# Kernel tuning notes

Measured on AMD Instinct MI355X. Metric: run time of the kernel, lower is better.

The kernel has to match this reference:

```python
import jax, jax.numpy as jnp
import numpy as np

HD = 128; ED = 64; V = 11; K = 64; L = 1024; LQ = 1024
EPS = 1e-5

def _ln(x, g, b):
    m = jnp.mean(x, axis=-1, keepdims=True)
    v = jnp.mean((x - m) ** 2, axis=-1, keepdims=True)
    return (x - m) / jnp.sqrt(v + EPS) * g + b

def _conv1d(x, w, b):
    # x: [B, C, L], w: [O, I, 3] (torch Conv1d layout), padding=1
    y = jax.lax.conv_general_dilated(x, w, (1,), [(1, 1)],
                                     dimension_numbers=("NCH", "OIH", "NCH"))
    return y + b[None, :, None]

def _enc(ids, emb, c1w, c1b, c2w, c2b, c3w, c3b, n1g, n1b, n2g, n2b, n3g, n3b):
    h = emb[ids].transpose(0, 2, 1)                      # [B, ED, L]
    h = jax.nn.relu(_conv1d(h, c1w, c1b)).transpose(0, 2, 1)
    h = _ln(h, n1g, n1b).transpose(0, 2, 1)
    h = jax.nn.relu(_conv1d(h, c2w, c2b)).transpose(0, 2, 1)
    h = _ln(h, n2g, n2b).transpose(0, 2, 1)
    h = jax.nn.relu(_conv1d(h, c3w, c3b)).transpose(0, 2, 1)
    return _ln(h, n3g, n3b)                              # [B, L, HD]

def setup_inputs() -> dict:
    key = jax.random.key(0)
    ks = iter(jax.random.split(key, 64))
    def nrm(shape, s=0.05):
        return (jax.random.normal(next(ks), shape, dtype=jnp.float32) * s)
    inp = {
        "support_inputs": jax.random.randint(next(ks), (K, L), 0, 10),
        "support_outputs": jax.random.randint(next(ks), (K, L), 0, 10),
        "query_input": jax.random.randint(next(ks), (LQ,), 0, 10),
    }
    for pre in ("qe", "se"):
        inp[pre + "_emb"] = nrm((V, ED)).at[10].set(0.0)
        inp[pre + "_c1w"] = nrm((HD, ED, 3)); inp[pre + "_c1b"] = nrm((HD,))
        inp[pre + "_c2w"] = nrm((HD, HD, 3)); inp[pre + "_c2b"] = nrm((HD,))
        inp[pre + "_c3w"] = nrm((HD, HD, 3)); inp[pre + "_c3b"] = nrm((HD,))
        for i in (1, 2, 3):
            inp[pre + f"_n{i}g"] = jnp.ones((HD,), jnp.float32)
            inp[pre + f"_n{i}b"] = jnp.zeros((HD,), jnp.float32)
    inp["out_emb"] = nrm((V, HD)).at[10].set(0.0)
    inp["dec_w1"] = nrm((HD, 2 * HD)); inp["dec_b1"] = nrm((HD,))
    inp["dec_lng"] = jnp.ones((HD,), jnp.float32)
    inp["dec_lnb"] = jnp.zeros((HD,), jnp.float32)
    inp["dec_w2"] = nrm((10, HD)); inp["dec_b2"] = nrm((10,))
    return inp

def reference(support_inputs, support_outputs, query_input,
              qe_emb, qe_c1w, qe_c1b, qe_c2w, qe_c2b, qe_c3w, qe_c3b,
              qe_n1g, qe_n1b, qe_n2g, qe_n2b, qe_n3g, qe_n3b,
              se_emb, se_c1w, se_c1b, se_c2w, se_c2b, se_c3w, se_c3b,
              se_n1g, se_n1b, se_n2g, se_n2b, se_n3g, se_n3b,
              out_emb, dec_w1, dec_b1, dec_lng, dec_lnb, dec_w2, dec_b2):
    q = _enc(query_input[None], qe_emb, qe_c1w, qe_c1b, qe_c2w, qe_c2b,
             qe_c3w, qe_c3b, qe_n1g, qe_n1b, qe_n2g, qe_n2b, qe_n3g, qe_n3b)[0]   # [LQ, HD]
    s = _enc(support_inputs, se_emb, se_c1w, se_c1b, se_c2w, se_c2b,
             se_c3w, se_c3b, se_n1g, se_n1b, se_n2g, se_n2b, se_n3g, se_n3b)      # [K, L, HD]
    keys = s.reshape(-1, HD)                              # [K*L, HD]
    values = out_emb[support_outputs].reshape(-1, HD)     # [K*L, HD]
    scores = (q @ keys.T) / jnp.sqrt(jnp.float32(HD))     # [LQ, K*L]
    attn = jax.nn.softmax(scores, axis=-1)
    attended = attn @ values                              # [LQ, HD]
    combined = jnp.concatenate([q, attended], axis=-1)    # [LQ, 2*HD]
    h = jax.nn.relu(combined @ dec_w1.T + dec_b1)
    h = _ln(h, dec_lng, dec_lnb)
    return h @ dec_w2.T + dec_b2                          # [LQ, 10]
```

## Files before the change

kernel.cpp:

```cpp
#include <hip/hip_runtime.h>


typedef __attribute__((ext_vector_type(8))) short short8;
typedef __attribute__((ext_vector_type(4))) float f32x4;
typedef __attribute__((ext_vector_type(4))) int int4v;
typedef __attribute__((ext_vector_type(4))) _Float16 half4;

#define EPSV 1e-5f
#define SC 0.12751676f

__device__ __forceinline__ float b2f(unsigned short u) {
  union { unsigned int i; float f; } v; v.i = ((unsigned int)u) << 16; return v.f;
}
__device__ __forceinline__ unsigned short f2b(float f) {
  union { float f; unsigned int i; } v; v.f = f;
  unsigned int r = v.i + 0x7fffu + ((v.i >> 16) & 1u);
  return (unsigned short)(r >> 16);
}
__device__ __forceinline__ f32x4 mfma32(short8 a, short8 b, f32x4 c) {
  return __builtin_amdgcn_mfma_f32_16x16x32_bf16(a, b, c, 0, 0, 0);
}
__device__ __forceinline__ f32x4 mfma16(half4 a, half4 b, f32x4 c) {
  return __builtin_amdgcn_mfma_f32_16x16x16f16(a, b, c, 0, 0, 0);
}
__device__ __forceinline__ void gl_lds16(const void* g, void* l) {
  __builtin_amdgcn_global_load_lds(
      (const __attribute__((address_space(1))) void*)g,
      (__attribute__((address_space(3))) void*)l, 16, 0, 0);
}
__device__ __forceinline__ half4 exp4_pk(f32x4 c) {
  float x0 = exp2f(c[0] * SC - 4.0f), x1 = exp2f(c[1] * SC - 4.0f);
  float x2 = exp2f(c[2] * SC - 4.0f), x3 = exp2f(c[3] * SC - 4.0f);
  union { __fp16 __attribute__((ext_vector_type(2))) h; unsigned int u; } a, b;
  a.h = __builtin_amdgcn_cvt_pkrtz(x0, x1);
  b.h = __builtin_amdgcn_cvt_pkrtz(x2, x3);
  union { unsigned int u[2]; half4 v; } r;
  r.u[0] = a.u; r.u[1] = b.u;
  return r.v;
}

#define OFF_WQ1 0
#define OFF_WQ2 24576
#define OFF_WQ3 73728
#define OFF_WS1 122880
#define OFF_WS2 147456
#define OFF_WS3 196608
#define OFF_EMBQ 245760
#define OFF_EMBS 246464
#define OFF_PBQ 247168
#define OFF_PBS 248320
#define OFF_OEMB 249472
#define OFF_DW1 250880
#define OFF_DB1 283648
#define OFF_DLNG 283776
#define OFF_DLNB 283904
#define OFF_DW2 284032
#define OFF_DB2 285312

__global__ __launch_bounds__(256) void mn_prep(
    const void* qc1w, const void* qc2w, const void* qc3w,
    const void* sc1w, const void* sc2w, const void* sc3w,
    const void* qemb, const void* semb,
    const void* qc1b, const void* qc2b, const void* qc3b,
    const void* qn1g, const void* qn1b, const void* qn2g, const void* qn2b,
    const void* qn3g, const void* qn3b,
    const void* sc1b, const void* sc2b, const void* sc3b,
    const void* sn1g, const void* sn1b, const void* sn2g, const void* sn2b,
    const void* sn3g, const void* sn3b,
    const void* oemb, const void* dw1, const void* db1, const void* dlng,
    const void* dlnb, const void* dw2, const void* db2,
    unsigned short* __restrict__ P, const unsigned int* __restrict__ det) {
  const bool f32m = (*det == 0x3F800000u);
  const int j = blockIdx.y;
  const void* src; int off, n, cin;
  switch (j) {
    case 0:  src = qc1w; off = OFF_WQ1; n = 24576; cin = 64; break;
    case 1:  src = qc2w; off = OFF_WQ2; n = 49152; cin = 128; break;
    case 2:  src = qc3w; off = OFF_WQ3; n = 49152; cin = 128; break;
    case 3:  src = sc1w; off = OFF_WS1; n = 24576; cin = 64; break;
    case 4:  src = sc2w; off = OFF_WS2; n = 49152; cin = 128; break;
    case 5:  src = sc3w; off = OFF_WS3; n = 49152; cin = 128; break;
    case 6:  src = qemb; off = OFF_EMBQ; n = 704; cin = 0; break;
    case 7:  src = semb; off = OFF_EMBS; n = 704; cin = 0; break;
    case 8:  src = qc1b; off = OFF_PBQ + 0; n = 128; cin = 0; break;
    case 9:  src = qc2b; off = OFF_PBQ + 128; n = 128; cin = 0; break;
    case 10: src = qc3b; off = OFF_PBQ + 256; n = 128; cin = 0; break;
    case 11: src = qn1g; off = OFF_PBQ + 384; n = 128; cin = 0; break;
    case 12: src = qn1b; off = OFF_PBQ + 512; n = 128; cin = 0; break;
    case 13: src = qn2g; off = OFF_PBQ + 640; n = 128; cin = 0; break;
    case 14: src = qn2b; off = OFF_PBQ + 768; n = 128; cin = 0; break;
    case 15: src = qn3g; off = OFF_PBQ + 896; n = 128; cin = 0; break;
    case 16: src = qn3b; off = OFF_PBQ + 1024; n = 128; cin = 0; break;
    case 17: src = sc1b; off = OFF_PBS + 0; n = 128; cin = 0; break;
    case 18: src = sc2b; off = OFF_PBS + 128; n = 128; cin = 0; break;
    case 19: src = sc3b; off = OFF_PBS + 256; n = 128; cin = 0; break;
    case 20: src = sn1g; off = OFF_PBS + 384; n = 128; cin = 0; break;
    case 21: src = sn1b; off = OFF_PBS + 512; n = 128; cin = 0; break;
    case 22: src = sn2g; off = OFF_PBS + 640; n = 128; cin = 0; break;
    case 23: src = sn2b; off = OFF_PBS + 768; n = 128; cin = 0; break;
    case 24: src = sn3g; off = OFF_PBS + 896; n = 128; cin = 0; break;
    case 25: src = sn3b; off = OFF_PBS + 1024; n = 128; cin = 0; break;
    case 26: src = oemb; off = OFF_OEMB; n = 1408; cin = 0; break;
    case 27: src = dw1; off = OFF_DW1; n = 32768; cin = 0; break;
    case 28: src = db1; off = OFF_DB1; n = 128; cin = 0; break;
    case 29: src = dlng; off = OFF_DLNG; n = 128; cin = 0; break;
    case 30: src = dlnb; off = OFF_DLNB; n = 128; cin = 0; break;
    case 31: src = dw2; off = OFF_DW2; n = 1280; cin = 0; break;
    default: src = db2; off = OFF_DB2; n = 10; cin = 0; break;
  }
  for (int e = blockIdx.x * 256 + threadIdx.x; e < n; e += gridDim.x * 256) {
    int si = e;
    if (cin) {
      int kw = 3 * cin;
      int o = e / kw, rem = e - o * kw;
      int c = rem >> 3, s = rem & 7;
      int k = ((c ^ (o & 7)) << 3) + s;
      int t = k / cin, i = k - t * cin;
      si = o * kw + i * 3 + t;
    }
    unsigned short v = f32m ? f2b(((const float*)src)[si]) : ((const unsigned short*)src)[si];
    P[off + e] = v;
  }
}

__global__ __launch_bounds__(256) void mn_gtf16(const int* __restrict__ so,
                                                unsigned short* __restrict__ gtf) {
  int t = blockIdx.x * 256 + threadIdx.x;
  int kb = t >> 6, l = t & 63;
  int id = l & 15, g = l >> 4;
  const int* base = so + kb * 16 + g * 4;
  half4 v;
#pragma unroll
  for (int j = 0; j < 4; ++j) {
    int s = base[j];
    bool on = (id < 11) ? (s == id) : (id == 11);
    v[j] = on ? (_Float16)1.0f : (_Float16)0.0f;
  }
  *(half4*)(gtf + (size_t)t * 4) = v;
}

template <int CIN, bool EMBED>
__global__ __launch_bounds__(256, 1) void mn_conv(
    const int* __restrict__ sup_ids, const int* __restrict__ q_ids,
    const unsigned short* __restrict__ in_act,
    const unsigned short* __restrict__ se_emb, const unsigned short* __restrict__ qe_emb,
    const unsigned short* __restrict__ se_wt, const unsigned short* __restrict__ qe_wt,
    const unsigned short* __restrict__ se_b, const unsigned short* __restrict__ qe_b,
    const unsigned short* __restrict__ se_g, const unsigned short* __restrict__ qe_g,
    const unsigned short* __restrict__ se_bt, const unsigned short* __restrict__ qe_bt,
    unsigned short* __restrict__ out_act) {
  constexpr int RB = CIN * 2;
  constexpr int KW = 3 * CIN;
  constexpr int RWB = KW * 2;
  constexpr int WB = 128 * RWB;
  constexpr int XB = 130 * RB;
  constexpr int NK = KW / 32;
  constexpr int WIT = WB / 4096;
  constexpr int CH = RB / 16;
  constexpr int NTASK = 130 * CH;
  constexpr int NT = (NTASK + 255) / 256;
  __shared__ __attribute__((aligned(16))) char lds[WB + XB + 4 * 4352];

  const int b = blockIdx.x;
  int first, nitems;
  if (b < 244)      { first = 2 * b;             nitems = 2; }
  else if (b < 252) { first = 488 + 3 * (b - 244); nitems = 3; }
  else              { first = 512 + 2 * (b - 252); nitems = 2; }
  const bool is_q = (first >= 512);

  const int tid = threadIdx.x;
  const int l = tid & 63, w = tid >> 6;
  const unsigned short* wt = is_q ? qe_wt : se_wt;
  const unsigned short* bs = is_q ? qe_b : se_b;
  const unsigned short* gg = is_q ? qe_g : se_g;
  const unsigned short* bt = is_q ? qe_bt : se_bt;
  const unsigned short* emb = is_q ? qe_emb : se_emb;
  char* xlds = lds + WB;

  {
    const char* wsrc = (const char*)wt + (size_t)(w * WIT) * 1024 + l * 16;
    char* wdst = lds + (w * WIT) * 1024;
#pragma unroll
    for (int i = 0; i < WIT; ++i) gl_lds16(wsrc + i * 1024, wdst + i * 1024);
  }

  int4v vals[NT];
  int dsto[NT];
#define XPHASE1(ITEM)                                                          \
  do {                                                                         \
    int _seq = (ITEM) >> 3, _t0 = ((ITEM) & 7) * 128;                          \
    const int* _ids = EMBED ? (is_q ? q_ids : (sup_ids + _seq * 1024)) : nullptr; \
    const unsigned short* _src = EMBED ? nullptr : in_act + (size_t)_seq * 1024 * CIN; \
    _Pragma("unroll") for (int i = 0; i < NT; ++i) {                           \
      int task = tid + i * 256;                                                \
      int r = task / CH, cb = (task % CH) * 16;                                \
      int p = _t0 + r - 1;                                                     \
      bool ok = (task < NTASK) && p >= 0 && p < 1024;                          \
      int4v v = {0, 0, 0, 0};                                                  \
      if constexpr (EMBED) {                                                   \
        if (ok) v = *(const int4v*)((const char*)emb + _ids[p] * RB + cb);     \
      } else {                                                                 \
        if (ok) v = *(const int4v*)((const char*)_src + (size_t)p * RB + cb);  \
      }                                                                        \
      vals[i] = v;                                                             \
      dsto[i] = (task < NTASK) ? (r * RB + (cb ^ ((r & 7) << 4))) : -1;        \
    }                                                                          \
  } while (0)
#define XPHASE2                                                                \
  do {                                                                         \
    _Pragma("unroll") for (int i = 0; i < NT; ++i)                             \
      if (dsto[i] >= 0) *(int4v*)(xlds + dsto[i]) = vals[i];                   \
  } while (0)

  XPHASE1(first);
  XPHASE2;
  asm volatile("s_waitcnt vmcnt(0)" ::: "memory");
  __syncthreads();

  const int g = l >> 4, q16 = l & 15;
  const int pbase = w * 32;

  float pb[8], pg[8], pt_[8];
#pragma unroll
  for (int ob = 0; ob < 8; ++ob) {
    int o = ob * 16 + q16;
    pb[ob] = b2f(bs[o]); pg[ob] = b2f(gg[o]); pt_[ob] = b2f(bt[o]);
  }
  char* wrep = lds + WB + XB + w * 4352;

  for (int s = 0; s < nitems; ++s) {
    const int item = first + s;
    const int seqI = item >> 3, t0I = (item & 7) * 128;

    f32x4 acc[2][8];
#pragma unroll
    for (int pt = 0; pt < 2; ++pt)
#pragma unroll
      for (int ob = 0; ob < 8; ++ob) acc[pt][ob] = (f32x4){0.f, 0.f, 0.f, 0.f};

#pragma unroll
    for (int ks = 0; ks < NK; ++ks) {
      const int kk = ks * 32;
      const int t = kk / CIN, i0 = kk % CIN;
      const int cb = (i0 + g * 8) * 2;
      short8 a0, a1;
      {
        int r = pbase + q16 + t;
        a0 = *(const short8*)(xlds + r * RB + (cb ^ ((r & 7) << 4)));
        r += 16;
        a1 = *(const short8*)(xlds + r * RB + (cb ^ ((r & 7) << 4)));
      }
      const int wc = ((ks * 4 + g) ^ (q16 & 7)) << 4;
#pragma unroll
      for (int ob = 0; ob < 8; ++ob) {
        short8 bb = *(const short8*)(lds + (ob * 16 + q16) * RWB + wc);
        acc[0][ob] = mfma32(a0, bb, acc[0][ob]);
        acc[1][ob] = mfma32(a1, bb, acc[1][ob]);
      }
    }
    __syncthreads();

    const bool more = (s + 1 < nitems);
    if (more) XPHASE1(item + 1);

#pragma unroll
    for (int pt = 0; pt < 2; ++pt) {
#pragma unroll
      for (int rg = 0; rg < 4; ++rg) {
        float v[8], sm = 0.f, sq = 0.f;
#pragma unroll
        for (int ob = 0; ob < 8; ++ob) {
          float x = acc[pt][ob][rg] + pb[ob];
          x = fmaxf(x, 0.f);
          v[ob] = x; sm += x; sq += x * x;
        }
#pragma unroll
        for (int m = 1; m < 16; m <<= 1) {
          sm += __shfl_xor(sm, m);
          sq += __shfl_xor(sq, m);
        }
        float mean = sm * (1.f / 128.f);
        float var = sq * (1.f / 128.f) - mean * mean;
        float rstd = rsqrtf(var + EPSV);
        unsigned short* dst = (unsigned short*)(wrep + (g * 4 + rg) * 272);
#pragma unroll
        for (int ob = 0; ob < 8; ++ob)
          dst[ob * 16 + q16] = f2b((v[ob] - mean) * rstd * pg[ob] + pt_[ob]);
      }
      char* obase = (char*)out_act + ((size_t)seqI * 1024 + t0I + pbase + pt * 16) * 256;
#pragma unroll
      for (int i = 0; i < 4; ++i) {
        int task = i * 64 + l;
        int pos = task >> 4, chk = task & 15;
        int4v v = *(const int4v*)(wrep + pos * 272 + chk * 16);
        *(int4v*)(obase + pos * 256 + chk * 16) = v;
      }
    }

    if (more) {
      XPHASE2;
      __syncthreads();
    }
  }
#undef XPHASE1
#undef XPHASE2
}

__global__ __launch_bounds__(256, 2) void mn_attn(const unsigned short* __restrict__ act3,
                                                  const unsigned short* __restrict__ gtf,
                                                  float* __restrict__ Hp) {
  __shared__ __attribute__((aligned(16))) char smem[27648];
  const int tid = threadIdx.x;
  const int l = tid & 63, w = tid >> 6;
  const int g = l >> 4, q16 = l & 15;
  const int ch = blockIdx.x;
  const int qt0 = (blockIdx.y * 4 + w) * 2;

  short8 qfa[4], qfb[4];
  const unsigned short* qrow = act3 + ((size_t)(64 * 1024 + qt0 * 16 + q16)) * 128;
#pragma unroll
  for (int ks = 0; ks < 4; ++ks) {
    qfa[ks] = *(const short8*)(qrow + ks * 32 + g * 8);
    qfb[ks] = *(const short8*)(qrow + 16 * 128 + ks * 32 + g * 8);
  }

  const char* kglob = (const char*)act3 + ((size_t)ch * 1024) * 256;
  const char* gglob = (const char*)gtf + ((size_t)ch * 64) * 512;

  int o0 = (w * 2) * 64 + l, o1 = (w * 2 + 1) * 64 + l;
  int r0s = o0 >> 4, c0s = (o0 & 15) ^ (r0s & 7);
  int r1s = o1 >> 4, c1s = (o1 & 15) ^ (r1s & 7);

#define STAGE(BUF, T)                                                          \
  do {                                                                         \
    const char* _gk = kglob + (size_t)(T) * 8192;                              \
    char* _lk = smem + (BUF) * 8192;                                           \
    gl_lds16(_gk + r0s * 256 + c0s * 16, _lk + (w * 2) * 1024);                \
    gl_lds16(_gk + r1s * 256 + c1s * 16, _lk + (w * 2 + 1) * 1024);            \
    if (w == 0)                                                                \
      gl_lds16(gglob + (size_t)(T) * 1024 + l * 16, smem + 24576 + (BUF) * 1024); \
  } while (0)
#define WAITSTAGE                                                              \
  do {                                                                         \
    if (w == 0) asm volatile("s_waitcnt vmcnt(3)" ::: "memory");               \
    else asm volatile("s_waitcnt vmcnt(2)" ::: "memory");                      \
  } while (0)

  int rc[4], rc1[4];
#pragma unroll
  for (int ks = 0; ks < 4; ++ks) {
    int c = (ks * 4 + g) ^ (q16 & 7);
    rc[ks] = q16 * 256 + c * 16;
    rc1[ks] = (16 + q16) * 256 + c * 16;
  }

  f32x4 hacca = {0.f, 0.f, 0.f, 0.f}, haccb = {0.f, 0.f, 0.f, 0.f};

  STAGE(0, 0);
  STAGE(1, 1);
  WAITSTAGE;
  __builtin_amdgcn_s_barrier();

  for (int it = 0; it < 32; ++it) {
    const int cur = it % 3;
    const char* kb = smem + cur * 8192;
    const char* gb = smem + 24576 + cur * 1024;

    short8 kc0[4], kc1[4];
#pragma unroll
    for (int ks = 0; ks < 4; ++ks) {
      kc0[ks] = *(const short8*)(kb + rc[ks]);
      kc1[ks] = *(const short8*)(kb + rc1[ks]);
    }

    f32x4 c0a = {0.f, 0.f, 0.f, 0.f}, c1a = {0.f, 0.f, 0.f, 0.f};
    f32x4 c0b = {0.f, 0.f, 0.f, 0.f}, c1b = {0.f, 0.f, 0.f, 0.f};
#pragma unroll
    for (int ks = 0; ks < 4; ++ks) {
      c0a = mfma32(kc0[ks], qfa[ks], c0a);
      c1a = mfma32(kc1[ks], qfa[ks], c1a);
      c0b = mfma32(kc0[ks], qfb[ks], c0b);
      c1b = mfma32(kc1[ks], qfb[ks], c1b);
    }

    half4 gf0 = *(const half4*)(gb + l * 8);
    half4 gf1 = *(const half4*)(gb + 512 + l * 8);

    hacca = mfma16(gf0, exp4_pk(c0a), hacca);
    hacca = mfma16(gf1, exp4_pk(c1a), hacca);
    haccb = mfma16(gf0, exp4_pk(c0b), haccb);
    haccb = mfma16(gf1, exp4_pk(c1b), haccb);

    if (it < 30) {
      STAGE((it + 2) % 3, it + 2);
      WAITSTAGE;
    } else {
      asm volatile("s_waitcnt vmcnt(0)" ::: "memory");
    }
    __builtin_amdgcn_s_barrier();
  }
#undef STAGE
#undef WAITSTAGE

  float* outa = Hp + ((size_t)(qt0 * 64 + ch) << 8) + q16;
  float* outb = Hp + ((size_t)((qt0 + 1) * 64 + ch) << 8) + q16;
#pragma unroll
  for (int rg = 0; rg < 4; ++rg) {
    outa[(g * 4 + rg) * 16] = hacca[rg];
    outb[(g * 4 + rg) * 16] = haccb[rg];
  }
}

__global__ __launch_bounds__(256) void mn_combine(const float* __restrict__ Hp,
                                                  const unsigned short* __restrict__ oemb,
                                                  float* __restrict__ att) {
  const int qt = blockIdx.x, tid = threadIdx.x;
  __shared__ float Hs[256];
  float s = 0.f;
  const float* base = Hp + (size_t)qt * 64 * 256 + tid;
  for (int ch = 0; ch < 64; ++ch) s += base[ch * 256];
  Hs[tid] = s;
  __syncthreads();
  for (int e = tid; e < 2048; e += 256) {
    int q = e >> 7, d = e & 127;
    float acc = 0.f;
#pragma unroll
    for (int id = 0; id < 11; ++id) acc += Hs[id * 16 + q] * b2f(oemb[id * 128 + d]);
    att[(size_t)(qt * 16 + q) * 128 + d] = acc / Hs[11 * 16 + q];
  }
}

__global__ __launch_bounds__(128) void mn_dec(
    const unsigned short* __restrict__ act3, const float* __restrict__ att,
    const unsigned short* __restrict__ P, void* __restrict__ out,
    const unsigned int* __restrict__ det) {
  const int row = blockIdx.x, o = threadIdx.x;
  const bool f32m = (*det == 0x3F800000u);
  __shared__ float c[256];
  __shared__ float yv[128];
  __shared__ float red[4];
  c[o] = b2f(act3[((size_t)(64 * 1024) + row) * 128 + o]);
  c[128 + o] = att[(size_t)row * 128 + o];
  __syncthreads();
  float acc = b2f(P[OFF_DB1 + o]);
  const unsigned short* wr = P + OFF_DW1 + o * 256;
  for (int k = 0; k < 256; k += 8) {
    short8 wv = *(const short8*)(wr + k);
#pragma unroll
    for (int j = 0; j < 8; ++j) acc += b2f((unsigned short)wv[j]) * c[k + j];
  }
  float h = fmaxf(acc, 0.f);
  float s = h, sq = h * h;
#pragma unroll
  for (int m = 1; m < 64; m <<= 1) { s += __shfl_xor(s, m); sq += __shfl_xor(sq, m); }
  int wid = o >> 6;
  if ((o & 63) == 0) { red[wid] = s; red[2 + wid] = sq; }
  __syncthreads();
  s = red[0] + red[1]; sq = red[2] + red[3];
  float mean = s * (1.f / 128.f);
  float var = sq * (1.f / 128.f) - mean * mean;
  float rstd = rsqrtf(var + EPSV);
  float y = (h - mean) * rstd * b2f(P[OFF_DLNG + o]) + b2f(P[OFF_DLNB + o]);
  yv[o] = y;
  __syncthreads();
  if (o < 10) {
    float a2 = b2f(P[OFF_DB2 + o]);
    const unsigned short* w2r = P + OFF_DW2 + o * 128;
    for (int k = 0; k < 128; ++k) a2 += b2f(w2r[k]) * yv[k];
    if (f32m) ((float*)out)[(size_t)row * 10 + o] = a2;
    else ((unsigned short*)out)[(size_t)row * 10 + o] = f2b(a2);
  }
}

extern "C" void kernel_launch(void* const* d_in, const int* in_sizes, int n_in,
                              void* d_out, int out_size, void* d_ws, size_t ws_size,
                              hipStream_t stream) {
  (void)in_sizes; (void)n_in; (void)out_size; (void)ws_size;
  const int* sup_in = (const int*)d_in[0];
  const int* sup_out = (const int*)d_in[1];
  const int* q_in = (const int*)d_in[2];

  char* ws = (char*)d_ws;
  unsigned short* P = (unsigned short*)ws;
  unsigned short* actA = (unsigned short*)(ws + 1048576);
  unsigned short* actB = (unsigned short*)(ws + 18087936);
  unsigned short* gtf = (unsigned short*)(ws + 35127296);
  float* Hp = (float*)(ws + 37224448);
  float* attb = (float*)(ws + 41418752);

  const unsigned int* det = (const unsigned int*)d_in[10];

  mn_prep<<<dim3(192, 33), 256, 0, stream>>>(
      d_in[4], d_in[6], d_in[8], d_in[17], d_in[19], d_in[21],
      d_in[3], d_in[16],
      d_in[5], d_in[7], d_in[9],
      d_in[10], d_in[11], d_in[12], d_in[13], d_in[14], d_in[15],
      d_in[18], d_in[20], d_in[22],
      d_in[23], d_in[24], d_in[25], d_in[26], d_in[27], d_in[28],
      d_in[29], d_in[30], d_in[31], d_in[32], d_in[33], d_in[34], d_in[35],
      P, det);
  mn_gtf16<<<1024, 256, 0, stream>>>(sup_out, gtf);
  mn_conv<64, true><<<256, 256, 0, stream>>>(
      sup_in, q_in, nullptr, P + OFF_EMBS, P + OFF_EMBQ, P + OFF_WS1, P + OFF_WQ1,
      P + OFF_PBS + 0, P + OFF_PBQ + 0, P + OFF_PBS + 384, P + OFF_PBQ + 384,
      P + OFF_PBS + 512, P + OFF_PBQ + 512, actA);
  mn_conv<128, false><<<256, 256, 0, stream>>>(
      nullptr, nullptr, actA, nullptr, nullptr, P + OFF_WS2, P + OFF_WQ2,
      P + OFF_PBS + 128, P + OFF_PBQ + 128, P + OFF_PBS + 640, P + OFF_PBQ + 640,
      P + OFF_PBS + 768, P + OFF_PBQ + 768, actB);
  mn_conv<128, false><<<256, 256, 0, stream>>>(
      nullptr, nullptr, actB, nullptr, nullptr, P + OFF_WS3, P + OFF_WQ3,
      P + OFF_PBS + 256, P + OFF_PBQ + 256, P + OFF_PBS + 896, P + OFF_PBQ + 896,
      P + OFF_PBS + 1024, P + OFF_PBQ + 1024, actA);
  mn_attn<<<dim3(64, 8), 256, 0, stream>>>(actA, gtf, Hp);
  mn_combine<<<64, 256, 0, stream>>>(Hp, P + OFF_OEMB, attb);
  mn_dec<<<1024, 128, 0, stream>>>(actA, attb, P, d_out, det);
}
```

Baseline: 124.8 us.

## Widen attention query tiles, prefetch conv inputs earlier, shrink prep grid

The attention kernel now gives each wave four 16-row query tiles instead of two, so each staged key/value chunk is reused across twice as many queries. The grid is halved and launch bounds relaxed to one block per SIMD to make room for the extra registers. The conv kernel issues the next item's input prefetch before the MFMA loop rather than after it, overlapping the load with compute. The prep launch grid is also reduced. The risks are higher register pressure and lower occupancy in attention, plus possibly fewer blocks than needed to cover prep's work if its loop does not stride.

New measurement: 133.4 us. 6.8% more time.

```diff
diff --git a/kernel.cpp b/kernel.cpp
--- a/kernel.cpp
+++ b/kernel.cpp
@@ -163,7 +163,7 @@
 
   const int b = blockIdx.x;
   int first, nitems;
-  if (b < 244)      { first = 2 * b;             nitems = 2; }
+  if (b < 244)      { first = 2 * b;               nitems = 2; }
   else if (b < 252) { first = 488 + 3 * (b - 244); nitems = 3; }
   else              { first = 512 + 2 * (b - 252); nitems = 2; }
   const bool is_q = (first >= 512);
@@ -231,6 +231,9 @@
   for (int s = 0; s < nitems; ++s) {
     const int item = first + s;
     const int seqI = item >> 3, t0I = (item & 7) * 128;
+    const bool more = (s + 1 < nitems);
+
+    if (more) XPHASE1(item + 1);
 
     f32x4 acc[2][8];
 #pragma unroll
@@ -260,8 +263,7 @@
     }
     __syncthreads();
 
-    const bool more = (s + 1 < nitems);
-    if (more) XPHASE1(item + 1);
+    if (more) XPHASE2;
 
 #pragma unroll
     for (int pt = 0; pt < 2; ++pt) {
@@ -297,16 +299,13 @@
       }
     }
 
-    if (more) {
-      XPHASE2;
-      __syncthreads();
-    }
+    if (more) __syncthreads();
   }
 #undef XPHASE1
 #undef XPHASE2
 }
 
-__global__ __launch_bounds__(256, 2) void mn_attn(const unsigned short* __restrict__ act3,
+__global__ __launch_bounds__(256, 1) void mn_attn(const unsigned short* __restrict__ act3,
                                                   const unsigned short* __restrict__ gtf,
                                                   float* __restrict__ Hp) {
   __shared__ __attribute__((aligned(16))) char smem[27648];
@@ -314,15 +313,15 @@
   const int l = tid & 63, w = tid >> 6;
   const int g = l >> 4, q16 = l & 15;
   const int ch = blockIdx.x;
-  const int qt0 = (blockIdx.y * 4 + w) * 2;
-
-  short8 qfa[4], qfb[4];
+  const int qt0 = blockIdx.y * 16 + w * 4;
+
+  short8 qf[4][4];
   const unsigned short* qrow = act3 + ((size_t)(64 * 1024 + qt0 * 16 + q16)) * 128;
 #pragma unroll
-  for (int ks = 0; ks < 4; ++ks) {
-    qfa[ks] = *(const short8*)(qrow + ks * 32 + g * 8);
-    qfb[ks] = *(const short8*)(qrow + 16 * 128 + ks * 32 + g * 8);
-  }
+  for (int t = 0; t < 4; ++t)
+#pragma unroll
+    for (int ks = 0; ks < 4; ++ks)
+      qf[t][ks] = *(const short8*)(qrow + t * 16 * 128 + ks * 32 + g * 8);
 
   const char* kglob = (const char*)act3 + ((size_t)ch * 1024) * 256;
   const char* gglob = (const char*)gtf + ((size_t)ch * 64) * 512;
@@ -354,7 +353,9 @@
     rc1[ks] = (16 + q16) * 256 + c * 16;
   }
 
-  f32x4 hacca = {0.f, 0.f, 0.f, 0.f}, haccb = {0.f, 0.f, 0.f, 0.f};
+  f32x4 hacc[4];
+#pragma unroll
+  for (int t = 0; t < 4; ++t) hacc[t] = (f32x4){0.f, 0.f, 0.f, 0.f};
 
   STAGE(0, 0);
   STAGE(1, 1);
@@ -373,23 +374,28 @@
       kc1[ks] = *(const short8*)(kb + rc1[ks]);
     }
 
-    f32x4 c0a = {0.f, 0.f, 0.f, 0.f}, c1a = {0.f, 0.f, 0.f, 0.f};
-    f32x4 c0b = {0.f, 0.f, 0.f, 0.f}, c1b = {0.f, 0.f, 0.f, 0.f};
-#pragma unroll
-    for (int ks = 0; ks < 4; ++ks) {
-      c0a = mfma32(kc0[ks], qfa[ks], c0a);
-      c1a = mfma32(kc1[ks], qfa[ks], c1a);
-      c0b = mfma32(kc0[ks], qfb[ks], c0b);
-      c1b = mfma32(kc1[ks], qfb[ks], c1b);
-    }
+    f32x4 s0[4], s1[4];
+#pragma unroll
+    for (int t = 0; t < 4; ++t) {
+      s0[t] = (f32x4){0.f, 0.f, 0.f, 0.f};
+      s1[t] = (f32x4){0.f, 0.f, 0.f, 0.f};
+    }
+#pragma unroll
+    for (int ks = 0; ks < 4; ++ks)
+#pragma unroll
+      for (int t = 0; t < 4; ++t) {
+        s0[t] = mfma32(kc0[ks], qf[t][ks], s0[t]);
+        s1[t] = mfma32(kc1[ks], qf[t][ks], s1[t]);
+      }
 
     half4 gf0 = *(const half4*)(gb + l * 8);
     half4 gf1 = *(const half4*)(gb + 512 + l * 8);
 
-    hacca = mfma16(gf0, exp4_pk(c0a), hacca);
-    hacca = mfma16(gf1, exp4_pk(c1a), hacca);
-    haccb = mfma16(gf0, exp4_pk(c0b), haccb);
-    haccb = mfma16(gf1, exp4_pk(c1b), haccb);
+#pragma unroll
+    for (int t = 0; t < 4; ++t) {
+      hacc[t] = mfma16(gf0, exp4_pk(s0[t]), hacc[t]);
+      hacc[t] = mfma16(gf1, exp4_pk(s1[t]), hacc[t]);
+    }
 
     if (it < 30) {
       STAGE((it + 2) % 3, it + 2);
@@ -402,12 +408,11 @@
 #undef STAGE
 #undef WAITSTAGE
 
-  float* outa = Hp + ((size_t)(qt0 * 64 + ch) << 8) + q16;
-  float* outb = Hp + ((size_t)((qt0 + 1) * 64 + ch) << 8) + q16;
-#pragma unroll
-  for (int rg = 0; rg < 4; ++rg) {
-    outa[(g * 4 + rg) * 16] = hacca[rg];
-    outb[(g * 4 + rg) * 16] = haccb[rg];
+#pragma unroll
+  for (int t = 0; t < 4; ++t) {
+    float* outp = Hp + ((size_t)((qt0 + t) * 64 + ch) << 8) + q16;
+#pragma unroll
+    for (int rg = 0; rg < 4; ++rg) outp[(g * 4 + rg) * 16] = hacc[t][rg];
   }
 }
 
@@ -490,7 +495,7 @@
 
   const unsigned int* det = (const unsigned int*)d_in[10];
 
-  mn_prep<<<dim3(192, 33), 256, 0, stream>>>(
+  mn_prep<<<dim3(48, 33), 256, 0, stream>>>(
       d_in[4], d_in[6], d_in[8], d_in[17], d_in[19], d_in[21],
       d_in[3], d_in[16],
       d_in[5], d_in[7], d_in[9],
@@ -512,7 +517,7 @@
       nullptr, nullptr, actB, nullptr, nullptr, P + OFF_WS3, P + OFF_WQ3,
       P + OFF_PBS + 256, P + OFF_PBQ + 256, P + OFF_PBS + 896, P + OFF_PBQ + 896,
       P + OFF_PBS + 1024, P + OFF_PBQ + 1024, actA);
-  mn_attn<<<dim3(64, 8), 256, 0, stream>>>(actA, gtf, Hp);
+  mn_attn<<<dim3(64, 4), 256, 0, stream>>>(actA, gtf, Hp);
   mn_combine<<<64, 256, 0, stream>>>(Hp, P + OFF_OEMB, attb);
   mn_dec<<<1024, 128, 0, stream>>>(actA, attb, P, d_out, det);
 }
```
